# Kernel optimization log

Measured on AMD Instinct MI355X. Metric: run time of the kernel, lower is better.

Reference implementation:

```python
import jax, jax.numpy as jnp
import numpy as np

N_NODES = 16000
N_EDGES = 256000
F = 128        # invariant edge feature dim
MUL = 64       # multiplicity of env/V irreps (mul_gcd)
HID = 128      # mlp_n_hidden
SQRT3 = float(np.sqrt(3.0))

# e3nn-style activation normalization constant for silu:
# c = sqrt(E_{z~N(0,1)}[silu(z)^2]), so silu(z)/c has unit second moment.
_z = np.linspace(-12.0, 12.0, 100001)
_pdf = np.exp(-0.5 * _z ** 2) / np.sqrt(2.0 * np.pi)
_silu = _z / (1.0 + np.exp(-_z))
SILU_C = float(np.sqrt(np.trapz(_silu ** 2 * _pdf, _z)))


def _nsilu(x):
    return jax.nn.silu(x) / SILU_C


def _lin(x, W):
    # e3nn 'path' gradient normalization: W ~ N(0,1), forward scaled by 1/sqrt(fan_in)
    return (x @ W) / jnp.sqrt(jnp.asarray(W.shape[0], x.dtype))


def setup_inputs() -> dict:
    key = jax.random.key(0)
    ks = jax.random.split(key, 11)
    inp = {
        'vectors': jax.random.normal(ks[0], (N_EDGES, 3), jnp.float32),
        'x': jax.random.normal(ks[1], (N_EDGES, F), jnp.float32),
        'V': jax.random.normal(ks[2], (N_EDGES, 4 * MUL), jnp.float32),  # 64x0e + 64x1o
        'u': jax.random.uniform(ks[3], (N_EDGES,), jnp.float32),
        'm': jnp.ones((N_EDGES,), jnp.float32),
        'W_env': jax.random.normal(ks[4], (F, 2 * MUL), jnp.float32),
        'W1': jax.random.normal(ks[5], (F + 2 * MUL, HID), jnp.float32),
        'W2': jax.random.normal(ks[6], (HID, HID), jnp.float32),
        'W3': jax.random.normal(ks[7], (HID, HID), jnp.float32),
        'W_out': jax.random.normal(ks[8], (2 * MUL, MUL), jnp.float32),
        'senders': jax.random.randint(ks[9], (N_EDGES,), 0, N_NODES, jnp.int32),
    }
    return inp


def reference(vectors, x, V, u, m, W_env, W1, W2, W3, W_out, senders):
    E = vectors.shape[0]
    x = x * m[:, None]

    # n_neighbors = scatter_sum(m, dst=senders, map_back=True)
    n_neighbors = jax.ops.segment_sum(m, senders, num_segments=N_NODES)[senders]  # (E,)

    # w = Linear(num_irreps=2*MUL)(x)
    w = _lin(x, W_env)                  # (E, 128)
    w0, w1 = w[:, :MUL], w[:, MUL:]     # scalar / vector channel weights

    # spherical harmonics (component normalization): Y0 = 1, Y1 = sqrt(3)*rhat
    rhat = vectors / jnp.linalg.norm(vectors, axis=-1, keepdims=True)
    Y1 = SQRT3 * rhat                   # (E, 3)

    # w * Y * m, scatter_sum over senders, map back, normalize by n_neighbors
    denom = n_neighbors + 1e-5
    ws = w0 * m[:, None]                                   # (E, MUL)   w * Y0
    wv = (w1[:, :, None] * Y1[:, None, :]) * m[:, None, None]  # (E, MUL, 3)
    wY_s = jax.ops.segment_sum(ws, senders, num_segments=N_NODES)[senders] / denom[:, None]
    wY_v = jax.ops.segment_sum(wv, senders, num_segments=N_NODES)[senders] / denom[:, None, None]

    # V.mul_to_axis(): (E, MUL, 0e+1o)
    Vs = V[:, :MUL]                      # (E, MUL)
    Vv = V[:, MUL:].reshape(E, MUL, 3)   # (E, MUL, 3)

    # tensor product, filter_ir_out = {0e, 1o} (CG, component normalization)
    s_a = wY_s * Vs                                  # 0e x 0e -> 0e
    s_b = jnp.sum(wY_v * Vv, axis=-1) / SQRT3        # 1o x 1o -> 0e
    v_a = wY_s[:, :, None] * Vv                      # 0e x 1o -> 1o
    v_b = wY_v * Vs[:, :, None]                      # 1o x 0e -> 1o

    # scalars -> concatenated into x; vectors stay equivariant
    x = jnp.concatenate([x, s_a, s_b], axis=1)       # (E, F + 2*MUL)

    # invariant MLP (silu, no output activation)
    h = _nsilu(_lin(x, W1))
    h = _nsilu(_lin(h, W2))
    h = _lin(h, W3)                                  # (E, HID)
    x_out = u[:, None] * h

    # Linear(irreps_out=64x1o) on 128x1o
    V_in = jnp.concatenate([v_a, v_b], axis=1)       # (E, 2*MUL, 3)
    V_out = jnp.einsum('euk,uo->eok', V_in, W_out) / jnp.sqrt(jnp.asarray(2 * MUL, V.dtype))
    V_out = V_out.reshape(E, MUL * 3)                # (E, 192)

    return x_out, V_out
```

## Files before the change

### kernel.cpp

```cpp
#include <hip/hip_runtime.h>
#include <math.h>

typedef short bf16x8 __attribute__((ext_vector_type(8)));
typedef float f32x4 __attribute__((ext_vector_type(4)));

#define S128 0.08838834764831845f
#define S256I 0.0625f
#define NN_NODES 16000

#define WS_COUNTS   16448000
#define WS_OFFSETS  (WS_COUNTS + 64000)
#define WS_CURSOR   (WS_OFFSETS + 64000)
#define WS_ORDER    (WS_CURSOR + 64000)
#define WS_W1 (WS_ORDER + 1024000)
#define WS_W2 (WS_W1 + 65536)
#define WS_W3 (WS_W2 + 32768)
#define WS_WO (WS_W3 + 32768)
#define WS_WE (WS_WO + 16384)

static float compute_inv_silu_c() {
    double sum = 0.0, prev = 0.0;
    const double dz = 24.0 / 100000.0;
    for (int i = 0; i <= 100000; ++i) {
        double z = -12.0 + dz * (double)i;
        double pdf = exp(-0.5 * z * z) * 0.3989422804014327;
        double s = z / (1.0 + exp(-z));
        double f = s * s * pdf;
        if (i) sum += 0.5 * (prev + f) * dz;
        prev = f;
    }
    return (float)(1.0 / sqrt(sum));
}
static const float INV_SILU_C = compute_inv_silu_c();

__device__ __forceinline__ unsigned int packbf(float a, float b) {
    union { float f; unsigned int u; } ca, cb;
    ca.f = a; cb.f = b;
    unsigned int ua = ca.u + (0x7fffu + ((ca.u >> 16) & 1u));
    unsigned int ub = cb.u + (0x7fffu + ((cb.u >> 16) & 1u));
    return (ua >> 16) | (ub & 0xffff0000u);
}
__device__ __forceinline__ unsigned short bf16r(float v) {
    union { float f; unsigned int u; } c; c.f = v;
    return (unsigned short)((c.u + (0x7fffu + ((c.u >> 16) & 1u))) >> 16);
}
__device__ __forceinline__ float bflo(unsigned int u) { return __uint_as_float(u << 16); }
__device__ __forceinline__ float bfhi(unsigned int u) { return __uint_as_float(u & 0xffff0000u); }
__device__ __forceinline__ int swz(int row, int b) { return b ^ ((row & 7) << 4); }
__device__ __forceinline__ float nsilu(float v, float ic) {
    return v / (1.0f + __expf(-v)) * ic;
}

__global__ __launch_bounds__(256) void k_wprep(
    const float* __restrict__ W1, const float* __restrict__ W2,
    const float* __restrict__ W3, const float* __restrict__ Wout,
    const float* __restrict__ Wenv, char* __restrict__ wsb)
{
    const int t = blockIdx.x * 256 + threadIdx.x;
    if (t < NN_NODES) ((int*)(wsb + WS_COUNTS))[t] = 0;
    if (t < 32768) {
        int n = t & 127, k = t >> 7;
        *(unsigned short*)(wsb + WS_W1 + n * 512 + k * 2) =
            bf16r(W1[k * 128 + n] * S256I);
    }
    if (t < 16384) {
        int n = t & 127, k = t >> 7;
        *(unsigned short*)(wsb + WS_W2 + n * 256 + k * 2) =
            bf16r(W2[k * 128 + n] * S128);
        *(unsigned short*)(wsb + WS_W3 + n * 256 + k * 2) =
            bf16r(W3[k * 128 + n] * S128);
    }
    if (t < 16384) {
        int j = t & 127, k = t >> 7;
        int c = (j & 1) ? 64 + (j >> 1) : (j >> 1);
        *(unsigned short*)(wsb + WS_WE + j * 256 + k * 2) =
            bf16r(Wenv[k * 128 + c] * S128);
    }
    if (t < 8192) {
        int o = t & 63, uu = t >> 6;
        *(unsigned short*)(wsb + WS_WO + o * 256 + ((uu * 2) ^ ((o & 7) << 4))) =
            bf16r(Wout[uu * 64 + o] * S128);
    }
}

__global__ __launch_bounds__(1024) void k_hist(
    const int* __restrict__ senders, int* __restrict__ counts, int E)
{
    const int e = blockIdx.x * 1024 + threadIdx.x;
    if (e < E) atomicAdd(&counts[senders[e]], 1);
}

__global__ __launch_bounds__(1024) void k_scan(
    const int* __restrict__ counts, int* __restrict__ offsets,
    int* __restrict__ cursor)
{
    __shared__ int part[1024];
    const int t = threadIdx.x;
    const int s0 = t * 16;
    const int s1 = (s0 + 16 < NN_NODES) ? s0 + 16 : NN_NODES;
    int s = 0;
    for (int i = s0; i < s1; ++i) s += counts[i];
    part[t] = s;
    __syncthreads();
    for (int off = 1; off < 1024; off <<= 1) {
        int v = part[t];
        if (t >= off) v += part[t - off];
        __syncthreads();
        part[t] = v;
        __syncthreads();
    }
    int run = t ? part[t - 1] : 0;
    for (int i = s0; i < s1; ++i) {
        offsets[i] = run; cursor[i] = run; run += counts[i];
    }
}

__global__ __launch_bounds__(1024) void k_binfill(
    const int* __restrict__ senders, int* __restrict__ cursor,
    int* __restrict__ order, int E)
{
    const int e = blockIdx.x * 1024 + threadIdx.x;
    if (e < E) {
        const int p = atomicAdd(&cursor[senders[e]], 1);
        order[p] = e;
    }
}

__global__ __launch_bounds__(512) void k_env(
    const float* __restrict__ x, const float* __restrict__ m,
    const char* __restrict__ wsb, char* __restrict__ wout, int E)
{
    __shared__ char lds[32768];
    const int tid = threadIdx.x, l = tid & 63, wid = tid >> 6;
    const int lr = l & 15, lg = l >> 4;
    const int n0 = wid * 16;

    bf16x8 B[4];
    #pragma unroll
    for (int kk = 0; kk < 4; ++kk)
        B[kk] = *(const bf16x8*)(wsb + WS_WE + (n0 + lr) * 256 + kk * 64 + lg * 16);

    const int eb = blockIdx.x * 128;
    {
        const int el = tid >> 2, q = tid & 3;
        const int e = eb + el;
        if (e < E) {
            const float mv = m[e];
            const float4* xp = (const float4*)&x[(size_t)e * 128 + q * 32];
            #pragma unroll
            for (int j = 0; j < 4; ++j) {
                float4 A = xp[2 * j], Bv = xp[2 * j + 1];
                int4 w;
                w.x = packbf(A.x * mv, A.y * mv); w.y = packbf(A.z * mv, A.w * mv);
                w.z = packbf(Bv.x * mv, Bv.y * mv); w.w = packbf(Bv.z * mv, Bv.w * mv);
                *(int4*)(lds + el * 256 + swz(el, q * 64 + j * 16)) = w;
            }
        } else {
            const int4 z = {0, 0, 0, 0};
            #pragma unroll
            for (int j = 0; j < 4; ++j)
                *(int4*)(lds + el * 256 + swz(el, q * 64 + j * 16)) = z;
        }
    }
    __syncthreads();

    f32x4 acc[8];
    #pragma unroll
    for (int a = 0; a < 8; ++a) acc[a] = (f32x4){0.f, 0.f, 0.f, 0.f};

    #pragma unroll
    for (int kk = 0; kk < 4; ++kk) {
        const int kb = kk * 64 + lg * 16;
        #pragma unroll
        for (int mt = 0; mt < 8; ++mt) {
            const int row = mt * 16 + lr;
            bf16x8 a = *(const bf16x8*)(lds + row * 256 + swz(row, kb));
            acc[mt] = __builtin_amdgcn_mfma_f32_16x16x32_bf16(a, B[kk], acc[mt], 0, 0, 0);
        }
    }
    __syncthreads();

    #pragma unroll
    for (int mt = 0; mt < 8; ++mt)
        #pragma unroll
        for (int r = 0; r < 4; ++r) {
            const int row = mt * 16 + lg * 4 + r;
            *(unsigned short*)(lds + row * 256 + (((n0 + lr) * 2) ^ ((row & 7) << 4))) =
                bf16r(acc[mt][r]);
        }
    __syncthreads();

    {
        const int el = tid >> 2, q = tid & 3;
        const int e = eb + el;
        if (e < E) {
            int4* d = (int4*)(wout + (size_t)e * 256 + q * 64);
            #pragma unroll
            for (int j = 0; j < 4; ++j)
                d[j] = *(int4*)(lds + el * 256 + ((q * 64 + j * 16) ^ ((el & 7) << 4)));
        }
    }
}

__global__ __launch_bounds__(256) void k_gather(
    const char* __restrict__ wvb, const float* __restrict__ vectors,
    const float* __restrict__ m, const int* __restrict__ counts,
    const int* __restrict__ offsets, const int* __restrict__ order,
    float* __restrict__ node_cnt, float* __restrict__ node_s,
    float* __restrict__ node_v)
{
    const int l = threadIdx.x & 63, wid = threadIdx.x >> 6;
    const int n = blockIdx.x * 4 + wid;
    if (n >= NN_NODES) return;
    const int cnt = counts[n], base = offsets[n];

    float as = 0.f, a0 = 0.f, a1 = 0.f, a2 = 0.f, am = 0.f;
    for (int i = 0; i < cnt; ++i) {
        const int e = order[base + i];
        const unsigned int wv = *(const unsigned int*)(wvb + (size_t)e * 256 + l * 4);
        const float mm = m[e];
        const float vx = vectors[(size_t)e * 3 + 0];
        const float vy = vectors[(size_t)e * 3 + 1];
        const float vz = vectors[(size_t)e * 3 + 2];
        const float rn = 1.7320508075688772f / sqrtf(vx * vx + vy * vy + vz * vz);
        const float w0 = bflo(wv) * mm;
        const float c1 = bfhi(wv) * mm * rn;
        as += w0; am += mm;
        a0 += c1 * vx; a1 += c1 * vy; a2 += c1 * vz;
    }
    if (l == 0) node_cnt[n] = am;
    node_s[(size_t)n * 64 + l] = as;
    float* nv = &node_v[((size_t)n * 64 + l) * 3];
    nv[0] = a0; nv[1] = a1; nv[2] = a2;
}

__global__ __launch_bounds__(512) void k_prep_vout(
    const float* __restrict__ V, const int* __restrict__ senders,
    const float* __restrict__ node_cnt, const float* __restrict__ node_s,
    const float* __restrict__ node_v, const char* __restrict__ wsb,
    float* __restrict__ out_x, float* __restrict__ out_v, int E)
{
    __shared__ char lds[49152 + 16384];
    const int tid = threadIdx.x, l = tid & 63, wid = tid >> 6;

    {
        const int4* src = (const int4*)(wsb + WS_WO);
        int4 a = src[tid * 2], b = src[tid * 2 + 1];
        ((int4*)(lds + 49152))[tid * 2]     = a;
        ((int4*)(lds + 49152))[tid * 2 + 1] = b;
    }

    const int eb = blockIdx.x * 64;
    #pragma unroll 2
    for (int i = 0; i < 8; ++i) {
        const int el = wid * 8 + i;
        const int e  = eb + el;
        float Vs = 0.f, Vv0 = 0.f, Vv1 = 0.f, Vv2 = 0.f;
        float wYs = 0.f, wv0 = 0.f, wv1 = 0.f, wv2 = 0.f;
        if (e < E) {
            Vs = V[(size_t)e * 256 + l];
            const float* vp = &V[(size_t)e * 256 + 64 + l * 3];
            Vv0 = vp[0]; Vv1 = vp[1]; Vv2 = vp[2];
            const int sn = senders[e];
            const float rden = 1.0f / (node_cnt[sn] + 1e-5f);
            wYs = node_s[(size_t)sn * 64 + l] * rden;
            const float* nvp = &node_v[((size_t)sn * 64 + l) * 3];
            wv0 = nvp[0] * rden; wv1 = nvp[1] * rden; wv2 = nvp[2] * rden;
            unsigned short* sab = (unsigned short*)((char*)out_x + (size_t)e * 512);
            sab[l]      = bf16r(wYs * Vs);
            sab[64 + l] = bf16r((wv0 * Vv0 + wv1 * Vv1 + wv2 * Vv2) * 0.57735026918962576f);
        }
        const float vvk[3] = {Vv0, Vv1, Vv2};
        const float wvk[3] = {wv0, wv1, wv2};
        #pragma unroll
        for (int k = 0; k < 3; ++k) {
            const int row = el * 3 + k;
            *(unsigned short*)(lds + row * 256 + swz(row, l * 2))       = bf16r(wYs * vvk[k]);
            *(unsigned short*)(lds + row * 256 + swz(row, 128 + l * 2)) = bf16r(wvk[k] * Vs);
        }
    }
    __syncthreads();

    const int wm = wid & 3, wn = wid >> 2;
    const int m0 = wm * 48, n0 = wn * 32;
    const int lr = l & 15, lg = l >> 4;
    f32x4 acc[3][2];
    #pragma unroll
    for (int a = 0; a < 3; ++a)
        #pragma unroll
        for (int b = 0; b < 2; ++b) acc[a][b] = (f32x4){0.f, 0.f, 0.f, 0.f};

    #pragma unroll
    for (int kk = 0; kk < 4; ++kk) {
        const int kb = kk * 64 + lg * 16;
        bf16x8 a0 = *(const bf16x8*)(lds + (m0 + lr) * 256      + swz(m0 + lr, kb));
        bf16x8 a1 = *(const bf16x8*)(lds + (m0 + 16 + lr) * 256 + swz(m0 + 16 + lr, kb));
        bf16x8 a2 = *(const bf16x8*)(lds + (m0 + 32 + lr) * 256 + swz(m0 + 32 + lr, kb));
        bf16x8 b0 = *(const bf16x8*)(lds + 49152 + (n0 + lr) * 256      + swz(n0 + lr, kb));
        bf16x8 b1 = *(const bf16x8*)(lds + 49152 + (n0 + 16 + lr) * 256 + swz(n0 + 16 + lr, kb));
        acc[0][0] = __builtin_amdgcn_mfma_f32_16x16x32_bf16(a0, b0, acc[0][0], 0, 0, 0);
        acc[0][1] = __builtin_amdgcn_mfma_f32_16x16x32_bf16(a0, b1, acc[0][1], 0, 0, 0);
        acc[1][0] = __builtin_amdgcn_mfma_f32_16x16x32_bf16(a1, b0, acc[1][0], 0, 0, 0);
        acc[1][1] = __builtin_amdgcn_mfma_f32_16x16x32_bf16(a1, b1, acc[1][1], 0, 0, 0);
        acc[2][0] = __builtin_amdgcn_mfma_f32_16x16x32_bf16(a2, b0, acc[2][0], 0, 0, 0);
        acc[2][1] = __builtin_amdgcn_mfma_f32_16x16x32_bf16(a2, b1, acc[2][1], 0, 0, 0);
    }
    __syncthreads();

    #pragma unroll
    for (int mt = 0; mt < 3; ++mt)
        #pragma unroll
        for (int nt = 0; nt < 2; ++nt)
            #pragma unroll
            for (int r = 0; r < 4; ++r) {
                const int mm = m0 + mt * 16 + lg * 4 + r;
                const int el2 = mm / 3, kd = mm - el2 * 3;
                const int o = n0 + nt * 16 + lr;
                *(float*)(lds + el2 * 768 + (o * 3 + kd) * 4) = acc[mt][nt][r];
            }
    __syncthreads();
    if (eb + 64 <= E) {
        const int4* s = (const int4*)lds;
        int4* d = (int4*)(out_v + (size_t)eb * 192);
        #pragma unroll
        for (int j = 0; j < 6; ++j) d[tid * 6 + j] = s[tid * 6 + j];
    } else {
        for (int idx = tid; idx < 64 * 192; idx += 512) {
            const int el2 = idx / 192;
            if (eb + el2 < E)
                out_v[(size_t)(eb + el2) * 192 + (idx % 192)] = *(float*)(lds + idx * 4);
        }
    }
}

__global__ __launch_bounds__(512, 4) void k_mlp(
    const float* __restrict__ x, const float* __restrict__ m,
    const float* __restrict__ ug, const char* __restrict__ wsb,
    float* __restrict__ out_x, float inv_c, int E)
{
    __shared__ char lds[49152];
    const int tid = threadIdx.x, l = tid & 63, wid = tid >> 6;
    const int lr = l & 15, lg = l >> 4;
    const int n0 = wid * 16;
    const int eb = blockIdx.x * 64;

    bf16x8 B1[8];
    #pragma unroll
    for (int kk = 0; kk < 8; ++kk)
        B1[kk] = *(const bf16x8*)(wsb + WS_W1 + (n0 + lr) * 512 + kk * 64 + lg * 16);

    {
        const int el = tid >> 3, q = tid & 7;
        const int e = eb + el;
        if (e < E) {
            const float mv = m[e];
            const float4* xp = (const float4*)&x[(size_t)e * 128 + q * 16];
            float4 A = xp[0], Bv = xp[1], C = xp[2], D = xp[3];
            int4 w0, w1;
            w0.x = packbf(A.x * mv, A.y * mv);   w0.y = packbf(A.z * mv, A.w * mv);
            w0.z = packbf(Bv.x * mv, Bv.y * mv); w0.w = packbf(Bv.z * mv, Bv.w * mv);
            w1.x = packbf(C.x * mv, C.y * mv);   w1.y = packbf(C.z * mv, C.w * mv);
            w1.z = packbf(D.x * mv, D.y * mv);   w1.w = packbf(D.z * mv, D.w * mv);
            *(int4*)(lds + el * 512 + swz(el, q * 32))      = w0;
            *(int4*)(lds + el * 512 + swz(el, q * 32 + 16)) = w1;
            const int4* sp = (const int4*)((const char*)out_x + (size_t)e * 512 + q * 32);
            *(int4*)(lds + el * 512 + swz(el, 256 + q * 32))      = sp[0];
            *(int4*)(lds + el * 512 + swz(el, 256 + q * 32 + 16)) = sp[1];
        } else {
            const int4 z = {0, 0, 0, 0};
            *(int4*)(lds + el * 512 + swz(el, q * 32))            = z;
            *(int4*)(lds + el * 512 + swz(el, q * 32 + 16))       = z;
            *(int4*)(lds + el * 512 + swz(el, 256 + q * 32))      = z;
            *(int4*)(lds + el * 512 + swz(el, 256 + q * 32 + 16)) = z;
        }
    }
    __syncthreads();

    f32x4 a1[4];
    #pragma unroll
    for (int a = 0; a < 4; ++a) a1[a] = (f32x4){0.f, 0.f, 0.f, 0.f};
    #pragma unroll
    for (int kk = 0; kk < 8; ++kk) {
        const int kb = kk * 64 + lg * 16;
        #pragma unroll
        for (int mt = 0; mt < 4; ++mt) {
            const int row = mt * 16 + lr;
            bf16x8 a = *(const bf16x8*)(lds + row * 512 + swz(row, kb));
            a1[mt] = __builtin_amdgcn_mfma_f32_16x16x32_bf16(a, B1[kk], a1[mt], 0, 0, 0);
        }
    }

    bf16x8 B2[4], B3[4];
    #pragma unroll
    for (int kk = 0; kk < 4; ++kk) {
        B2[kk] = *(const bf16x8*)(wsb + WS_W2 + (n0 + lr) * 256 + kk * 64 + lg * 16);
        B3[kk] = *(const bf16x8*)(wsb + WS_W3 + (n0 + lr) * 256 + kk * 64 + lg * 16);
    }

    #pragma unroll
    for (int mt = 0; mt < 4; ++mt)
        #pragma unroll
        for (int r = 0; r < 4; ++r) {
            const int row = mt * 16 + lg * 4 + r;
            *(unsigned short*)(lds + 32768 + row * 256 + swz(row, (n0 + lr) * 2)) =
                bf16r(nsilu(a1[mt][r], inv_c));
        }
    __syncthreads();

    f32x4 a2[4];
    #pragma unroll
    for (int a = 0; a < 4; ++a) a2[a] = (f32x4){0.f, 0.f, 0.f, 0.f};
    #pragma unroll
    for (int kk = 0; kk < 4; ++kk) {
        const int kb = kk * 64 + lg * 16;
        #pragma unroll
        for (int mt = 0; mt < 4; ++mt) {
            const int row = mt * 16 + lr;
            bf16x8 a = *(const bf16x8*)(lds + 32768 + row * 256 + swz(row, kb));
            a2[mt] = __builtin_amdgcn_mfma_f32_16x16x32_bf16(a, B2[kk], a2[mt], 0, 0, 0);
        }
    }
    #pragma unroll
    for (int mt = 0; mt < 4; ++mt)
        #pragma unroll
        for (int r = 0; r < 4; ++r) {
            const int row = mt * 16 + lg * 4 + r;
            *(unsigned short*)(lds + row * 256 + swz(row, (n0 + lr) * 2)) =
                bf16r(nsilu(a2[mt][r], inv_c));
        }
    __syncthreads();

    f32x4 a3[4];
    #pragma unroll
    for (int a = 0; a < 4; ++a) a3[a] = (f32x4){0.f, 0.f, 0.f, 0.f};
    #pragma unroll
    for (int kk = 0; kk < 4; ++kk) {
        const int kb = kk * 64 + lg * 16;
        #pragma unroll
        for (int mt = 0; mt < 4; ++mt) {
            const int row = mt * 16 + lr;
            bf16x8 a = *(const bf16x8*)(lds + row * 256 + swz(row, kb));
            a3[mt] = __builtin_amdgcn_mfma_f32_16x16x32_bf16(a, B3[kk], a3[mt], 0, 0, 0);
        }
    }
    __syncthreads();

    #pragma unroll
    for (int mt = 0; mt < 4; ++mt)
        #pragma unroll
        for (int r = 0; r < 4; ++r) {
            const int row = mt * 16 + lg * 4 + r;
            *(float*)(lds + row * 512 + (((n0 + lr) * 4) ^ ((row & 7) << 4))) = a3[mt][r];
        }
    __syncthreads();

    {
        const int el = tid >> 3, q = tid & 7;
        const int e = eb + el;
        if (e < E) {
            const float uu = ug[e];
            #pragma unroll
            for (int j = 0; j < 4; ++j) {
                int4 v = *(int4*)(lds + el * 512 + ((q * 64 + j * 16) ^ ((el & 7) << 4)));
                float4 f;
                f.x = __int_as_float(v.x) * uu; f.y = __int_as_float(v.y) * uu;
                f.z = __int_as_float(v.z) * uu; f.w = __int_as_float(v.w) * uu;
                *(float4*)(&out_x[(size_t)e * 128 + q * 16 + j * 4]) = f;
            }
        }
    }
}

extern "C" void kernel_launch(void* const* d_in, const int* in_sizes, int n_in,
                              void* d_out, int out_size, void* d_ws, size_t ws_size,
                              hipStream_t stream) {
    const float* vectors = (const float*)d_in[0];
    const float* x       = (const float*)d_in[1];
    const float* V       = (const float*)d_in[2];
    const float* u       = (const float*)d_in[3];
    const float* m       = (const float*)d_in[4];
    const float* W_env   = (const float*)d_in[5];
    const float* W1      = (const float*)d_in[6];
    const float* W2      = (const float*)d_in[7];
    const float* W3      = (const float*)d_in[8];
    const float* W_out   = (const float*)d_in[9];
    const int*   senders = (const int*)d_in[10];

    const int E = in_sizes[4];

    char*  wsb      = (char*)d_ws;
    float* node_cnt = (float*)d_ws;
    float* node_s   = node_cnt + NN_NODES;
    float* node_v   = node_s + (size_t)NN_NODES * 64;
    int* counts  = (int*)(wsb + WS_COUNTS);
    int* offsets = (int*)(wsb + WS_OFFSETS);
    int* cursor  = (int*)(wsb + WS_CURSOR);
    int* order   = (int*)(wsb + WS_ORDER);

    float* out_x = (float*)d_out;
    float* out_v = out_x + (size_t)E * 128;
    char*  wvb   = (char*)out_v;

    k_wprep<<<128, 256, 0, stream>>>(W1, W2, W3, W_out, W_env, wsb);
    k_hist<<<(E + 1023) / 1024, 1024, 0, stream>>>(senders, counts, E);
    k_scan<<<1, 1024, 0, stream>>>(counts, offsets, cursor);
    k_binfill<<<(E + 1023) / 1024, 1024, 0, stream>>>(senders, cursor, order, E);
    k_env<<<(E + 127) / 128, 512, 0, stream>>>(x, m, wsb, wvb, E);
    k_gather<<<(NN_NODES + 3) / 4, 256, 0, stream>>>(wvb, vectors, m, counts,
                                                     offsets, order,
                                                     node_cnt, node_s, node_v);
    k_prep_vout<<<(E + 63) / 64, 512, 0, stream>>>(V, senders, node_cnt, node_s,
                                                   node_v, wsb, out_x, out_v, E);
    k_mlp<<<(E + 63) / 64, 512, 0, stream>>>(x, m, u, wsb, out_x, INV_SILU_C, E);
}
```

Measured before the change: 455.3 us.

## Scatter env weights into sender-sorted order and cache bf16 masked x

k_binfill now records each edge's sorted position and writes packed (vector, mask) float4 records in sorted order. k_env scatters its weight rows to that sorted position, so k_gather reads contiguous rows with no order indirection or random loads of vectors and m. k_env also saves the masked bf16 x to workspace so k_mlp loads half the bytes and skips re-converting. The trade-off is extra workspace writes, a scattered write pattern in k_env, and extra traffic in binfill.

Result: no change. 448.5 us (-1.5%).

```diff
diff --git a/kernel.cpp b/kernel.cpp
--- a/kernel.cpp
+++ b/kernel.cpp
@@ -11,12 +11,14 @@
 #define WS_COUNTS   16448000
 #define WS_OFFSETS  (WS_COUNTS + 64000)
 #define WS_CURSOR   (WS_OFFSETS + 64000)
-#define WS_ORDER    (WS_CURSOR + 64000)
-#define WS_W1 (WS_ORDER + 1024000)
+#define WS_INV      (WS_CURSOR + 64000)
+#define WS_W1 (WS_INV + 1024000)
 #define WS_W2 (WS_W1 + 65536)
 #define WS_W3 (WS_W2 + 32768)
 #define WS_WO (WS_W3 + 32768)
 #define WS_WE (WS_WO + 16384)
+#define WS_VECM (WS_WE + 32768)
+#define WS_XMB  (WS_VECM + 4096000)
 
 static float compute_inv_silu_c() {
     double sum = 0.0, prev = 0.0;
@@ -116,19 +118,27 @@
 }
 
 __global__ __launch_bounds__(1024) void k_binfill(
-    const int* __restrict__ senders, int* __restrict__ cursor,
-    int* __restrict__ order, int E)
+    const int* __restrict__ senders, const float* __restrict__ vectors,
+    const float* __restrict__ m, int* __restrict__ cursor,
+    int* __restrict__ inv, float4* __restrict__ vecm, int E)
 {
     const int e = blockIdx.x * 1024 + threadIdx.x;
     if (e < E) {
         const int p = atomicAdd(&cursor[senders[e]], 1);
-        order[p] = e;
+        inv[e] = p;
+        float4 vm;
+        vm.x = vectors[(size_t)e * 3 + 0];
+        vm.y = vectors[(size_t)e * 3 + 1];
+        vm.z = vectors[(size_t)e * 3 + 2];
+        vm.w = m[e];
+        vecm[p] = vm;
     }
 }
 
 __global__ __launch_bounds__(512) void k_env(
     const float* __restrict__ x, const float* __restrict__ m,
-    const char* __restrict__ wsb, char* __restrict__ wout, int E)
+    const char* __restrict__ wsb, const int* __restrict__ inv,
+    char* __restrict__ wout, char* __restrict__ xmb, int E)
 {
     __shared__ char lds[32768];
     const int tid = threadIdx.x, l = tid & 63, wid = tid >> 6;
@@ -164,6 +174,17 @@
     }
     __syncthreads();
 
+    {
+        const int el = tid >> 2, q = tid & 3;
+        const int e = eb + el;
+        if (e < E) {
+            int4* d = (int4*)(xmb + (size_t)e * 256 + q * 64);
+            #pragma unroll
+            for (int j = 0; j < 4; ++j)
+                d[j] = *(int4*)(lds + el * 256 + ((q * 64 + j * 16) ^ ((el & 7) << 4)));
+        }
+    }
+
     f32x4 acc[8];
     #pragma unroll
     for (int a = 0; a < 8; ++a) acc[a] = (f32x4){0.f, 0.f, 0.f, 0.f};
@@ -194,7 +215,8 @@
         const int el = tid >> 2, q = tid & 3;
         const int e = eb + el;
         if (e < E) {
-            int4* d = (int4*)(wout + (size_t)e * 256 + q * 64);
+            const int p = inv[e];
+            int4* d = (int4*)(wout + (size_t)p * 256 + q * 64);
             #pragma unroll
             for (int j = 0; j < 4; ++j)
                 d[j] = *(int4*)(lds + el * 256 + ((q * 64 + j * 16) ^ ((el & 7) << 4)));
@@ -203,9 +225,8 @@
 }
 
 __global__ __launch_bounds__(256) void k_gather(
-    const char* __restrict__ wvb, const float* __restrict__ vectors,
-    const float* __restrict__ m, const int* __restrict__ counts,
-    const int* __restrict__ offsets, const int* __restrict__ order,
+    const char* __restrict__ wvb, const float4* __restrict__ vecm,
+    const int* __restrict__ counts, const int* __restrict__ offsets,
     float* __restrict__ node_cnt, float* __restrict__ node_s,
     float* __restrict__ node_v)
 {
@@ -216,17 +237,15 @@
 
     float as = 0.f, a0 = 0.f, a1 = 0.f, a2 = 0.f, am = 0.f;
     for (int i = 0; i < cnt; ++i) {
-        const int e = order[base + i];
-        const unsigned int wv = *(const unsigned int*)(wvb + (size_t)e * 256 + l * 4);
-        const float mm = m[e];
-        const float vx = vectors[(size_t)e * 3 + 0];
-        const float vy = vectors[(size_t)e * 3 + 1];
-        const float vz = vectors[(size_t)e * 3 + 2];
-        const float rn = 1.7320508075688772f / sqrtf(vx * vx + vy * vy + vz * vz);
-        const float w0 = bflo(wv) * mm;
-        const float c1 = bfhi(wv) * mm * rn;
-        as += w0; am += mm;
-        a0 += c1 * vx; a1 += c1 * vy; a2 += c1 * vz;
+        const unsigned int wv =
+            *(const unsigned int*)(wvb + (size_t)(base + i) * 256 + l * 4);
+        const float4 vm = vecm[base + i];
+        const float rn = 1.7320508075688772f /
+                         sqrtf(vm.x * vm.x + vm.y * vm.y + vm.z * vm.z);
+        const float w0 = bflo(wv) * vm.w;
+        const float c1 = bfhi(wv) * vm.w * rn;
+        as += w0; am += vm.w;
+        a0 += c1 * vm.x; a1 += c1 * vm.y; a2 += c1 * vm.z;
     }
     if (l == 0) node_cnt[n] = am;
     node_s[(size_t)n * 64 + l] = as;
@@ -334,9 +353,9 @@
 }
 
 __global__ __launch_bounds__(512, 4) void k_mlp(
-    const float* __restrict__ x, const float* __restrict__ m,
-    const float* __restrict__ ug, const char* __restrict__ wsb,
-    float* __restrict__ out_x, float inv_c, int E)
+    const char* __restrict__ xmb, const float* __restrict__ ug,
+    const char* __restrict__ wsb, float* __restrict__ out_x,
+    float inv_c, int E)
 {
     __shared__ char lds[49152];
     const int tid = threadIdx.x, l = tid & 63, wid = tid >> 6;
@@ -353,16 +372,9 @@
         const int el = tid >> 3, q = tid & 7;
         const int e = eb + el;
         if (e < E) {
-            const float mv = m[e];
-            const float4* xp = (const float4*)&x[(size_t)e * 128 + q * 16];
-            float4 A = xp[0], Bv = xp[1], C = xp[2], D = xp[3];
-            int4 w0, w1;
-            w0.x = packbf(A.x * mv, A.y * mv);   w0.y = packbf(A.z * mv, A.w * mv);
-            w0.z = packbf(Bv.x * mv, Bv.y * mv); w0.w = packbf(Bv.z * mv, Bv.w * mv);
-            w1.x = packbf(C.x * mv, C.y * mv);   w1.y = packbf(C.z * mv, C.w * mv);
-            w1.z = packbf(D.x * mv, D.y * mv);   w1.w = packbf(D.z * mv, D.w * mv);
-            *(int4*)(lds + el * 512 + swz(el, q * 32))      = w0;
-            *(int4*)(lds + el * 512 + swz(el, q * 32 + 16)) = w1;
+            const int4* xp = (const int4*)(xmb + (size_t)e * 256 + q * 32);
+            *(int4*)(lds + el * 512 + swz(el, q * 32))      = xp[0];
+            *(int4*)(lds + el * 512 + swz(el, q * 32 + 16)) = xp[1];
             const int4* sp = (const int4*)((const char*)out_x + (size_t)e * 512 + q * 32);
             *(int4*)(lds + el * 512 + swz(el, 256 + q * 32))      = sp[0];
             *(int4*)(lds + el * 512 + swz(el, 256 + q * 32 + 16)) = sp[1];
@@ -495,7 +507,9 @@
     int* counts  = (int*)(wsb + WS_COUNTS);
     int* offsets = (int*)(wsb + WS_OFFSETS);
     int* cursor  = (int*)(wsb + WS_CURSOR);
-    int* order   = (int*)(wsb + WS_ORDER);
+    int* inv     = (int*)(wsb + WS_INV);
+    float4* vecm = (float4*)(wsb + WS_VECM);
+    char* xmb    = wsb + WS_XMB;
 
     float* out_x = (float*)d_out;
     float* out_v = out_x + (size_t)E * 128;
@@ -504,12 +518,12 @@
     k_wprep<<<128, 256, 0, stream>>>(W1, W2, W3, W_out, W_env, wsb);
     k_hist<<<(E + 1023) / 1024, 1024, 0, stream>>>(senders, counts, E);
     k_scan<<<1, 1024, 0, stream>>>(counts, offsets, cursor);
-    k_binfill<<<(E + 1023) / 1024, 1024, 0, stream>>>(senders, cursor, order, E);
-    k_env<<<(E + 127) / 128, 512, 0, stream>>>(x, m, wsb, wvb, E);
-    k_gather<<<(NN_NODES + 3) / 4, 256, 0, stream>>>(wvb, vectors, m, counts,
-                                                     offsets, order,
+    k_binfill<<<(E + 1023) / 1024, 1024, 0, stream>>>(senders, vectors, m,
+                                                      cursor, inv, vecm, E);
+    k_env<<<(E + 127) / 128, 512, 0, stream>>>(x, m, wsb, inv, wvb, xmb, E);
+    k_gather<<<(NN_NODES + 3) / 4, 256, 0, stream>>>(wvb, vecm, counts, offsets,
                                                      node_cnt, node_s, node_v);
     k_prep_vout<<<(E + 63) / 64, 512, 0, stream>>>(V, senders, node_cnt, node_s,
                                                    node_v, wsb, out_x, out_v, E);
-    k_mlp<<<(E + 63) / 64, 512, 0, stream>>>(x, m, u, wsb, out_x, INV_SILU_C, E);
-}
+    k_mlp<<<(E + 63) / 64, 512, 0, stream>>>(xmb, u, wsb, out_x, INV_SILU_C, E);
+}
```
